# Optimization experiments

Measured on AMD Instinct MI355X. Metric: run time of the kernel, lower is better.

Reference implementation:

```python
import jax, jax.numpy as jnp
import numpy as np


def _safe_norm(x, eps=1e-8):
    return jnp.sqrt(jnp.clip(jnp.sum(x * x, axis=-1, keepdims=True), eps))


def _normalize(x, eps=1e-8):
    return x / _safe_norm(x, eps)


def _safe_direction(primary, fallback, eps=1e-6):
    bad = _safe_norm(primary, eps) < eps  # [N,1] bool
    out = jnp.where(bad, fallback, primary)
    return _normalize(out, eps)


def _build_frames(x):
    # x: [N,3] (N >= 2). Returns per-node rotation frames [N,3,3] (columns = axes).
    d = x[1:] - x[:-1]
    prev = jnp.concatenate([d[:1], d], axis=0)
    nxt = jnp.concatenate([d, d[-1:]], axis=0)
    tangent = _safe_direction(prev + nxt, nxt)
    curvature = _safe_direction(nxt - prev, prev)
    ay_raw = curvature - tangent * jnp.sum(curvature * tangent, axis=-1, keepdims=True)
    ay = _safe_direction(ay_raw, jnp.cross(tangent, prev))
    az = _safe_direction(jnp.cross(tangent, ay), jnp.cross(tangent, curvature))
    ay = _safe_direction(jnp.cross(az, tangent), ay)
    return jnp.stack([tangent, ay, az], axis=-1)


def setup_inputs() -> dict:
    key = jax.random.key(0)
    N, H, EH = 1024, 256, 128  # EH = max(16, H//2)
    ks = jax.random.split(key, 16)

    def lin(k, fi, fo):
        k1, k2 = jax.random.split(k)
        lim = 1.0 / np.sqrt(fi)
        W = jax.random.uniform(k1, (fi, fo), minval=-lim, maxval=lim, dtype=jnp.float32)
        b = jax.random.uniform(k2, (fo,), minval=-lim, maxval=lim, dtype=jnp.float32)
        return W, b

    h = jax.random.normal(ks[0], (N, H), dtype=jnp.float32)
    x_cond = jnp.cumsum(jax.random.normal(ks[1], (N, 3), dtype=jnp.float32) * 1.5, axis=0)
    x_t = x_cond + 0.05 * jax.random.normal(ks[2], (N, 3), dtype=jnp.float32)
    tau = jax.random.uniform(ks[3], (1,), dtype=jnp.float32)
    W_np1, b_np1 = lin(ks[4], H + 6, H)
    W_np2, b_np2 = lin(ks[5], H, H)
    w_src, b_src = lin(ks[6], H, 1)
    w_dst, b_dst = lin(ks[7], H, 1)
    w_ns, b_ns = lin(ks[8], H, 1)
    W_eg1, b_eg1 = lin(ks[9], 4, EH)
    w_eg2, b_eg2 = lin(ks[10], EH, 1)
    W_out1, b_out1 = lin(ks[11], H + 6, H)
    W_out2, b_out2 = lin(ks[12], H, 3)
    return dict(h=h, x_t=x_t, x_cond=x_cond, tau=tau,
                W_np1=W_np1, b_np1=b_np1, W_np2=W_np2, b_np2=b_np2,
                w_src=w_src, b_src=b_src, w_dst=w_dst, b_dst=b_dst,
                w_ns=w_ns, b_ns=b_ns, W_eg1=W_eg1, b_eg1=b_eg1,
                w_eg2=w_eg2, b_eg2=b_eg2, W_out1=W_out1, b_out1=b_out1,
                W_out2=W_out2, b_out2=b_out2)


def reference(h, x_t, x_cond, tau,
              W_np1, b_np1, W_np2, b_np2,
              w_src, b_src, w_dst, b_dst,
              w_ns, b_ns, W_eg1, b_eg1, w_eg2, b_eg2,
              W_out1, b_out1, W_out2, b_out2):
    silu = jax.nn.silu
    n = x_t.shape[0]
    frames = _build_frames(x_cond)                       # [N,3,3]
    delta = x_t - x_cond
    delta_local = jnp.einsum('nji,nj->ni', frames, delta)  # frames^T @ delta
    t = tau.reshape(())
    t_emb = jnp.broadcast_to(jnp.stack([t, jnp.sin(t), jnp.cos(t)]), (n, 3))
    node_feat = jnp.concatenate([h, delta_local, t_emb], axis=-1)
    nh = silu(node_feat @ W_np1 + b_np1)
    nh = silu(nh @ W_np2 + b_np2)                        # [N,H]
    # pairwise local geometry: rel[n,m] = x[m] - x[n], rotated into node n's frame
    rel = x_t[None, :, :] - x_t[:, None, :]              # [N,N,3]
    rel_local = jnp.einsum('nji,nmj->nmi', frames, rel)  # [N,N,3]
    dist = jnp.linalg.norm(rel_local, axis=-1, keepdims=True)
    edge_feat = jnp.concatenate([rel_local, dist], axis=-1)  # [N,N,4]
    eh = silu(edge_feat @ W_eg1 + b_eg1)                 # [N,N,EH]
    edge_logit = (eh @ w_eg2 + b_eg2)[..., 0]            # [N,N]
    src = nh @ w_src + b_src                             # [N,1] -> broadcast over m
    dst = (nh @ w_dst + b_dst)[:, 0]                     # [N]
    logits = src + dst[None, :] + edge_logit             # [N,N]
    diag = jnp.eye(n, dtype=bool)
    logits = jnp.where(diag, -10000.0, logits)
    attn = jax.nn.softmax(logits, axis=1)
    attn = jnp.where(diag, 0.0, attn)
    attn = attn / jnp.clip(jnp.sum(attn, axis=1, keepdims=True), 1e-6)
    ns = jax.nn.sigmoid(nh @ w_ns + b_ns)[:, 0]          # [N]
    msgs = jnp.einsum('nm,m,nmi->ni', attn, ns, rel_local)  # [N,3]
    uf = jnp.concatenate([nh, delta_local, msgs], axis=-1)
    local_update = silu(uf @ W_out1 + b_out1) @ W_out2 + b_out2
    vel_local = local_update + 0.25 * msgs
    return jnp.einsum('nij,nj->ni', frames, vel_local)
```

## Files before the change

### kernel.cpp

```cpp
#include <hip/hip_runtime.h>
#include <math.h>

#define DEV __device__ __forceinline__

typedef float v2f __attribute__((ext_vector_type(2)));
DEV v2f splat2(float s){ return (v2f){s, s}; }

struct F3 { float x, y, z; };

DEV F3 mkf3(float x, float y, float z){ F3 r; r.x=x; r.y=y; r.z=z; return r; }
DEV F3 f3add(F3 a, F3 b){ return mkf3(a.x+b.x, a.y+b.y, a.z+b.z); }
DEV F3 f3sub(F3 a, F3 b){ return mkf3(a.x-b.x, a.y-b.y, a.z-b.z); }
DEV F3 f3scale(F3 a, float s){ return mkf3(a.x*s, a.y*s, a.z*s); }
DEV float f3dot(F3 a, F3 b){ return a.x*b.x + a.y*b.y + a.z*b.z; }
DEV F3 f3cross(F3 a, F3 b){
  return mkf3(a.y*b.z - a.z*b.y, a.z*b.x - a.x*b.z, a.x*b.y - a.y*b.x);
}
DEV F3 f3dir(F3 v){
  float ss = f3dot(v, v);
  float inv = 1.0f / sqrtf(fmaxf(ss, 1e-6f));
  return f3scale(v, inv);
}
DEV float fast_silu(float x){
  return x * __builtin_amdgcn_rcpf(1.0f + __expf(-x));
}
DEV float fast_sigmoid(float x){
  return __builtin_amdgcn_rcpf(1.0f + __expf(-x));
}

__global__ void frames_kernel(const float* __restrict__ xc,
                              const float* __restrict__ xt,
                              float* __restrict__ frames,
                              float* __restrict__ dl,
                              const float* __restrict__ W_eg1,
                              const float* __restrict__ b_eg1,
                              const float* __restrict__ w_eg2,
                              float* __restrict__ wpk, int N)
{
  if (blockIdx.x == (unsigned)(N / 256)) {
    int j = threadIdx.x;
    if (j < 128) {
      const float nl2e = -1.44269504088896340736f;
      const float nln2 = -0.69314718055994530942f;
      wpk[j*8+0] = nl2e * W_eg1[j];
      wpk[j*8+1] = nl2e * W_eg1[128 + j];
      wpk[j*8+2] = nl2e * W_eg1[256 + j];
      wpk[j*8+3] = nl2e * W_eg1[384 + j];
      wpk[j*8+4] = nl2e * b_eg1[j];
      wpk[j*8+5] = nln2 * w_eg2[j];
      wpk[j*8+6] = 0.f; wpk[j*8+7] = 0.f;
    } else if (j < 144) {
      wpk[1024 + (j - 128)] = 0.f;
    }
    return;
  }
  int n = blockIdx.x * blockDim.x + threadIdx.x;
  if (n >= N) return;
  int pn = (n > 0) ? n - 1 : 0;
  int qn = (n < N - 1) ? n : N - 2;
  F3 prev = mkf3(xc[(pn+1)*3+0]-xc[pn*3+0], xc[(pn+1)*3+1]-xc[pn*3+1], xc[(pn+1)*3+2]-xc[pn*3+2]);
  F3 nxt  = mkf3(xc[(qn+1)*3+0]-xc[qn*3+0], xc[(qn+1)*3+1]-xc[qn*3+1], xc[(qn+1)*3+2]-xc[qn*3+2]);

  F3 tangent = f3dir(f3add(prev, nxt));
  F3 curv    = f3dir(f3sub(nxt, prev));
  float ct   = f3dot(curv, tangent);
  F3 ay      = f3dir(f3sub(curv, f3scale(tangent, ct)));
  F3 az      = f3dir(f3cross(tangent, ay));
  ay         = f3dir(f3cross(az, tangent));

  float* fr = frames + n * 9;
  fr[0] = tangent.x; fr[1] = ay.x; fr[2] = az.x;
  fr[3] = tangent.y; fr[4] = ay.y; fr[5] = az.y;
  fr[6] = tangent.z; fr[7] = ay.z; fr[8] = az.z;

  F3 delta = mkf3(xt[n*3+0]-xc[n*3+0], xt[n*3+1]-xc[n*3+1], xt[n*3+2]-xc[n*3+2]);
  dl[n*3+0] = f3dot(tangent, delta);
  dl[n*3+1] = f3dot(ay, delta);
  dl[n*3+2] = f3dot(az, delta);
}

__global__ __launch_bounds__(256) void node_mlp(
    const float* __restrict__ h, const float* __restrict__ dl,
    const float* __restrict__ tau,
    const float* __restrict__ W1, const float* __restrict__ b1,
    const float* __restrict__ W2, const float* __restrict__ b2,
    const float* __restrict__ w_src, const float* __restrict__ b_src,
    const float* __restrict__ w_dst, const float* __restrict__ b_dst,
    const float* __restrict__ w_ns, const float* __restrict__ b_ns,
    float* __restrict__ nh, float* __restrict__ srcv,
    float* __restrict__ dstv, float* __restrict__ nsv, int N)
{
  const int n0 = blockIdx.x * 4, tid = threadIdx.x;
  __shared__ float4 fA[262];
  __shared__ float4 fB[256];
  __shared__ float red[4][4][3];

  {
    const float* hp = h + n0 * 256 + tid;
    fA[tid] = make_float4(hp[0], hp[256], hp[512], hp[768]);
  }
  if (tid < 6) {
    int k = 256 + tid;
    float4 v;
    if (tid < 3) {
      v = make_float4(dl[(n0+0)*3+tid], dl[(n0+1)*3+tid],
                      dl[(n0+2)*3+tid], dl[(n0+3)*3+tid]);
    } else {
      float t = tau[0];
      float s = (tid == 3) ? t : ((tid == 4) ? sinf(t) : cosf(t));
      v = make_float4(s, s, s, s);
    }
    fA[k] = v;
  }
  __syncthreads();

  {
    float bb = b1[tid];
    float a0 = bb, a1 = bb, a2 = bb, a3 = bb;
    const float* Wp = W1 + tid;
    for (int kb = 0; kb < 256; kb += 64) {
      float w[64];
      #pragma unroll
      for (int u = 0; u < 64; ++u) w[u] = Wp[(kb + u) * 256];
      #pragma unroll
      for (int u = 0; u < 64; ++u) {
        float4 f = fA[kb + u];
        a0 = fmaf(f.x, w[u], a0); a1 = fmaf(f.y, w[u], a1);
        a2 = fmaf(f.z, w[u], a2); a3 = fmaf(f.w, w[u], a3);
      }
    }
    #pragma unroll
    for (int k = 256; k < 262; ++k) {
      float w = Wp[k * 256];
      float4 f = fA[k];
      a0 = fmaf(f.x, w, a0); a1 = fmaf(f.y, w, a1);
      a2 = fmaf(f.z, w, a2); a3 = fmaf(f.w, w, a3);
    }
    fB[tid] = make_float4(fast_silu(a0), fast_silu(a1), fast_silu(a2), fast_silu(a3));
  }
  __syncthreads();

  float bb = b2[tid];
  float a0 = bb, a1 = bb, a2 = bb, a3 = bb;
  const float* Wp = W2 + tid;
  for (int kb = 0; kb < 256; kb += 64) {
    float w[64];
    #pragma unroll
    for (int u = 0; u < 64; ++u) w[u] = Wp[(kb + u) * 256];
    #pragma unroll
    for (int u = 0; u < 64; ++u) {
      float4 f = fB[kb + u];
      a0 = fmaf(f.x, w[u], a0); a1 = fmaf(f.y, w[u], a1);
      a2 = fmaf(f.z, w[u], a2); a3 = fmaf(f.w, w[u], a3);
    }
  }

  const float wsv = w_src[tid], wdv = w_dst[tid], wnv = w_ns[tid];
  const int wave = tid >> 6, lane = tid & 63;
  float va[4] = {fast_silu(a0), fast_silu(a1), fast_silu(a2), fast_silu(a3)};
  #pragma unroll
  for (int r = 0; r < 4; ++r) {
    nh[(n0 + r) * 256 + tid] = va[r];
    float ps = va[r] * wsv, pd = va[r] * wdv, pn = va[r] * wnv;
    for (int off = 32; off; off >>= 1) {
      ps += __shfl_down(ps, off);
      pd += __shfl_down(pd, off);
      pn += __shfl_down(pn, off);
    }
    if (lane == 0) { red[wave][r][0] = ps; red[wave][r][1] = pd; red[wave][r][2] = pn; }
  }
  __syncthreads();
  if (tid < 4) {
    int r = tid;
    float s0 = 0.f, s1 = 0.f, s2 = 0.f;
    #pragma unroll
    for (int w = 0; w < 4; ++w) { s0 += red[w][r][0]; s1 += red[w][r][1]; s2 += red[w][r][2]; }
    srcv[n0 + r] = s0 + b_src[0];
    dstv[n0 + r] = s1 + b_dst[0];
    nsv[n0 + r]  = fast_sigmoid(s2 + b_ns[0]);
  }
}

__global__ __launch_bounds__(256) void edge_softmax(
    const float* __restrict__ x_t, const float* __restrict__ frames,
    const float* __restrict__ srcv, const float* __restrict__ dstv,
    const float* __restrict__ nsv,
    const float* __restrict__ wpk, const float* __restrict__ b_eg2,
    float* __restrict__ msgs, int N)
{
  const int n = blockIdx.x, tid = threadIdx.x;
  __shared__ float redmax[4];
  __shared__ float red[4][4];

  const float f0 = frames[n*9+0], f1 = frames[n*9+1], f2 = frames[n*9+2],
              f3_ = frames[n*9+3], f4 = frames[n*9+4], f5 = frames[n*9+5],
              f6 = frames[n*9+6], f7 = frames[n*9+7], f8 = frames[n*9+8];
  const float x0 = x_t[n*3+0], x1 = x_t[n*3+1], x2 = x_t[n*3+2];
  const float sn = srcv[n];
  const float b2v = b_eg2[0];

  float r0s[4], r1s[4], r2s[4], dds[4];
  #pragma unroll
  for (int e = 0; e < 4; ++e) {
    const int m = e * 256 + tid;
    float rx = x_t[m * 3 + 0] - x0;
    float ry = x_t[m * 3 + 1] - x1;
    float rz = x_t[m * 3 + 2] - x2;
    r0s[e] = f0 * rx + f3_ * ry + f6 * rz;
    r1s[e] = f1 * rx + f4 * ry + f7 * rz;
    r2s[e] = f2 * rx + f5 * ry + f8 * rz;
    dds[e] = sqrtf(r0s[e]*r0s[e] + r1s[e]*r1s[e] + r2s[e]*r2s[e]);
  }
  const v2f r0A = {r0s[0], r0s[1]}, r0B = {r0s[2], r0s[3]};
  const v2f r1A = {r1s[0], r1s[1]}, r1B = {r1s[2], r1s[3]};
  const v2f r2A = {r2s[0], r2s[1]}, r2B = {r2s[2], r2s[3]};
  const v2f ddA = {dds[0], dds[1]}, ddB = {dds[2], dds[3]};

  v2f accA = {0.f, 0.f}, accB = {0.f, 0.f};

  const float4* __restrict__ wp4 = (const float4*)wpk;

#define J_STEP(WA, WB)                                                    \
  {                                                                       \
    v2f tpA = splat2(WB.x) + splat2(WA.w) * ddA;                          \
    tpA += splat2(WA.z) * r2A;                                            \
    tpA += splat2(WA.y) * r1A;                                            \
    tpA += splat2(WA.x) * r0A;                                            \
    v2f tpB = splat2(WB.x) + splat2(WA.w) * ddB;                          \
    tpB += splat2(WA.z) * r2B;                                            \
    tpB += splat2(WA.y) * r1B;                                            \
    tpB += splat2(WA.x) * r0B;                                            \
    v2f eA, eB;                                                           \
    eA.x = __builtin_amdgcn_exp2f(tpA.x); eA.y = __builtin_amdgcn_exp2f(tpA.y); \
    eB.x = __builtin_amdgcn_exp2f(tpB.x); eB.y = __builtin_amdgcn_exp2f(tpB.y); \
    v2f opA = eA + splat2(1.0f);                                          \
    v2f opB = eB + splat2(1.0f);                                          \
    v2f sgA, sgB;                                                         \
    sgA.x = __builtin_amdgcn_rcpf(opA.x); sgA.y = __builtin_amdgcn_rcpf(opA.y); \
    sgB.x = __builtin_amdgcn_rcpf(opB.x); sgB.y = __builtin_amdgcn_rcpf(opB.y); \
    accA += (splat2(WB.y) * tpA) * sgA;                                   \
    accB += (splat2(WB.y) * tpB) * sgB;                                   \
  }

  float4 ca0 = wp4[0], cb0 = wp4[1], ca1 = wp4[2], cb1 = wp4[3];
  for (int c = 0; c < 64; ++c) {
    float4 na0 = wp4[(c + 1) * 4 + 0];
    float4 nb0 = wp4[(c + 1) * 4 + 1];
    float4 na1 = wp4[(c + 1) * 4 + 2];
    float4 nb1 = wp4[(c + 1) * 4 + 3];
    J_STEP(ca0, cb0)
    J_STEP(ca1, cb1)
    ca0 = na0; cb0 = nb0; ca1 = na1; cb1 = nb1;
  }
#undef J_STEP

  float l[4];
  float lmax = -3.4e38f;
  float accs[4] = {accA.x, accA.y, accB.x, accB.y};
  #pragma unroll
  for (int e = 0; e < 4; ++e) {
    const int m = e * 256 + tid;
    float lg = sn + dstv[m] + b2v + accs[e];
    if (m == n) lg = -10000.0f;
    l[e] = lg;
    lmax = fmaxf(lmax, lg);
  }

  for (int off = 32; off; off >>= 1) lmax = fmaxf(lmax, __shfl_down(lmax, off));
  const int wave = tid >> 6, lane = tid & 63;
  if (lane == 0) redmax[wave] = lmax;
  __syncthreads();
  const float mx = fmaxf(fmaxf(redmax[0], redmax[1]), fmaxf(redmax[2], redmax[3]));

  float r0all[4] = {r0A.x, r0A.y, r0B.x, r0B.y};
  float r1all[4] = {r1A.x, r1A.y, r1B.x, r1B.y};
  float r2all[4] = {r2A.x, r2A.y, r2B.x, r2B.y};
  float sum = 0.f, a0 = 0.f, a1 = 0.f, a2 = 0.f;
  #pragma unroll
  for (int e = 0; e < 4; ++e) {
    const int m = e * 256 + tid;
    float ee = __expf(l[e] - mx);
    sum += ee;
    float w = ee * nsv[m];
    a0 = fmaf(w, r0all[e], a0);
    a1 = fmaf(w, r1all[e], a1);
    a2 = fmaf(w, r2all[e], a2);
  }
  for (int off = 32; off; off >>= 1) {
    sum += __shfl_down(sum, off);
    a0 += __shfl_down(a0, off);
    a1 += __shfl_down(a1, off);
    a2 += __shfl_down(a2, off);
  }
  if (lane == 0) { red[wave][0] = sum; red[wave][1] = a0; red[wave][2] = a1; red[wave][3] = a2; }
  __syncthreads();
  if (tid == 0) {
    float Z  = red[0][0] + red[1][0] + red[2][0] + red[3][0];
    float m0 = red[0][1] + red[1][1] + red[2][1] + red[3][1];
    float m1 = red[0][2] + red[1][2] + red[2][2] + red[3][2];
    float m2 = red[0][3] + red[1][3] + red[2][3] + red[3][3];
    float invZ = 1.0f / Z;
    msgs[n * 3 + 0] = m0 * invZ;
    msgs[n * 3 + 1] = m1 * invZ;
    msgs[n * 3 + 2] = m2 * invZ;
  }
}

__global__ __launch_bounds__(256) void out_mlp(
    const float* __restrict__ nh, const float* __restrict__ dl,
    const float* __restrict__ msgs, const float* __restrict__ frames,
    const float* __restrict__ W1, const float* __restrict__ b1,
    const float* __restrict__ W2, const float* __restrict__ b2,
    float* __restrict__ out, int N)
{
  const int n0 = blockIdx.x * 4, tid = threadIdx.x;
  __shared__ float4 feat4[262];
  __shared__ float red[4][4][3];
  {
    const float* hp = nh + n0 * 256 + tid;
    feat4[tid] = make_float4(hp[0], hp[256], hp[512], hp[768]);
  }
  if (tid < 6) {
    int k = 256 + tid;
    float4 v;
    if (tid < 3) {
      v = make_float4(dl[(n0+0)*3+tid], dl[(n0+1)*3+tid],
                      dl[(n0+2)*3+tid], dl[(n0+3)*3+tid]);
    } else {
      int c = tid - 3;
      v = make_float4(msgs[(n0+0)*3+c], msgs[(n0+1)*3+c],
                      msgs[(n0+2)*3+c], msgs[(n0+3)*3+c]);
    }
    feat4[k] = v;
  }
  __syncthreads();

  float bb = b1[tid];
  float a0 = bb, a1 = bb, a2 = bb, a3 = bb;
  const float* Wp = W1 + tid;
  for (int kb = 0; kb < 256; kb += 64) {
    float w[64];
    #pragma unroll
    for (int u = 0; u < 64; ++u) w[u] = Wp[(kb + u) * 256];
    #pragma unroll
    for (int u = 0; u < 64; ++u) {
      float4 f = feat4[kb + u];
      a0 = fmaf(f.x, w[u], a0); a1 = fmaf(f.y, w[u], a1);
      a2 = fmaf(f.z, w[u], a2); a3 = fmaf(f.w, w[u], a3);
    }
  }
  #pragma unroll
  for (int k = 256; k < 262; ++k) {
    float w = Wp[k * 256];
    float4 f = feat4[k];
    a0 = fmaf(f.x, w, a0); a1 = fmaf(f.y, w, a1);
    a2 = fmaf(f.z, w, a2); a3 = fmaf(f.w, w, a3);
  }

  const float w0 = W2[tid * 3 + 0], w1 = W2[tid * 3 + 1], w2 = W2[tid * 3 + 2];
  const int wave = tid >> 6, lane = tid & 63;
  float va[4] = {fast_silu(a0), fast_silu(a1), fast_silu(a2), fast_silu(a3)};
  #pragma unroll
  for (int r = 0; r < 4; ++r) {
    float p0 = va[r] * w0, p1 = va[r] * w1, p2 = va[r] * w2;
    for (int off = 32; off; off >>= 1) {
      p0 += __shfl_down(p0, off);
      p1 += __shfl_down(p1, off);
      p2 += __shfl_down(p2, off);
    }
    if (lane == 0) { red[wave][r][0] = p0; red[wave][r][1] = p1; red[wave][r][2] = p2; }
  }
  __syncthreads();
  if (tid < 4) {
    int r = tid, n = n0 + r;
    float s0 = 0.f, s1 = 0.f, s2 = 0.f;
    #pragma unroll
    for (int w = 0; w < 4; ++w) { s0 += red[w][r][0]; s1 += red[w][r][1]; s2 += red[w][r][2]; }
    float m0 = msgs[n * 3 + 0], m1 = msgs[n * 3 + 1], m2 = msgs[n * 3 + 2];
    float v0 = s0 + b2[0] + 0.25f * m0;
    float v1 = s1 + b2[1] + 0.25f * m1;
    float v2 = s2 + b2[2] + 0.25f * m2;
    const float* fr = frames + n * 9;
    out[n * 3 + 0] = fr[0] * v0 + fr[1] * v1 + fr[2] * v2;
    out[n * 3 + 1] = fr[3] * v0 + fr[4] * v1 + fr[5] * v2;
    out[n * 3 + 2] = fr[6] * v0 + fr[7] * v1 + fr[8] * v2;
  }
}

extern "C" void kernel_launch(void* const* d_in, const int* in_sizes, int n_in,
                              void* d_out, int out_size, void* d_ws, size_t ws_size,
                              hipStream_t stream) {
  const float* h      = (const float*)d_in[0];
  const float* x_t    = (const float*)d_in[1];
  const float* x_cond = (const float*)d_in[2];
  const float* tau    = (const float*)d_in[3];
  const float* W_np1  = (const float*)d_in[4];
  const float* b_np1  = (const float*)d_in[5];
  const float* W_np2  = (const float*)d_in[6];
  const float* b_np2  = (const float*)d_in[7];
  const float* w_src  = (const float*)d_in[8];
  const float* b_src  = (const float*)d_in[9];
  const float* w_dst  = (const float*)d_in[10];
  const float* b_dst  = (const float*)d_in[11];
  const float* w_ns   = (const float*)d_in[12];
  const float* b_ns   = (const float*)d_in[13];
  const float* W_eg1  = (const float*)d_in[14];
  const float* b_eg1  = (const float*)d_in[15];
  const float* w_eg2  = (const float*)d_in[16];
  const float* b_eg2  = (const float*)d_in[17];
  const float* W_out1 = (const float*)d_in[18];
  const float* b_out1 = (const float*)d_in[19];
  const float* W_out2 = (const float*)d_in[20];
  const float* b_out2 = (const float*)d_in[21];
  float* out = (float*)d_out;

  const int N = in_sizes[1] / 3;

  float* ws     = (float*)d_ws;
  float* frames = ws;
  float* dl     = frames + N * 9;
  float* nh     = dl + N * 3;
  float* srcv   = nh + N * 256;
  float* dstv   = srcv + N;
  float* nsv    = dstv + N;
  float* msgs   = nsv + N;
  float* wpk    = msgs + N * 3;

  frames_kernel<<<N / 256 + 1, 256, 0, stream>>>(x_cond, x_t, frames, dl,
                                                 W_eg1, b_eg1, w_eg2, wpk, N);
  node_mlp<<<N / 4, 256, 0, stream>>>(h, dl, tau, W_np1, b_np1, W_np2, b_np2,
                                      w_src, b_src, w_dst, b_dst, w_ns, b_ns,
                                      nh, srcv, dstv, nsv, N);
  edge_softmax<<<N, 256, 0, stream>>>(x_t, frames, srcv, dstv, nsv,
                                      wpk, b_eg2, msgs, N);
  out_mlp<<<N / 4, 256, 0, stream>>>(nh, dl, msgs, frames,
                                     W_out1, b_out1, W_out2, b_out2, out, N);
}
```

Baseline: 65.07 us.

## Fuse frame construction and weight packing into node MLP kernel

Removes the separate frames_kernel launch by computing per-node frames and local deltas inside node_mlp (four threads per block) and packing the edge-MLP weights in block 0. The local deltas go through shared memory instead of a global round trip. In edge_softmax, dstv and nsv are loaded early into registers, and the inner loop uses explicit packed FMAs instead of separate multiply and add. This saves one kernel launch and a dependency at the cost of a small serial prologue plus an extra barrier in every node_mlp block.

```diff
diff --git a/kernel.cpp b/kernel.cpp
--- a/kernel.cpp
+++ b/kernel.cpp
@@ -5,6 +5,7 @@
 
 typedef float v2f __attribute__((ext_vector_type(2)));
 DEV v2f splat2(float s){ return (v2f){s, s}; }
+DEV v2f pkfma(v2f a, v2f b, v2f c){ return __builtin_elementwise_fma(a, b, c); }
 
 struct F3 { float x, y, z; };
 
@@ -28,65 +29,18 @@
   return __builtin_amdgcn_rcpf(1.0f + __expf(-x));
 }
 
-__global__ void frames_kernel(const float* __restrict__ xc,
-                              const float* __restrict__ xt,
-                              float* __restrict__ frames,
-                              float* __restrict__ dl,
-                              const float* __restrict__ W_eg1,
-                              const float* __restrict__ b_eg1,
-                              const float* __restrict__ w_eg2,
-                              float* __restrict__ wpk, int N)
-{
-  if (blockIdx.x == (unsigned)(N / 256)) {
-    int j = threadIdx.x;
-    if (j < 128) {
-      const float nl2e = -1.44269504088896340736f;
-      const float nln2 = -0.69314718055994530942f;
-      wpk[j*8+0] = nl2e * W_eg1[j];
-      wpk[j*8+1] = nl2e * W_eg1[128 + j];
-      wpk[j*8+2] = nl2e * W_eg1[256 + j];
-      wpk[j*8+3] = nl2e * W_eg1[384 + j];
-      wpk[j*8+4] = nl2e * b_eg1[j];
-      wpk[j*8+5] = nln2 * w_eg2[j];
-      wpk[j*8+6] = 0.f; wpk[j*8+7] = 0.f;
-    } else if (j < 144) {
-      wpk[1024 + (j - 128)] = 0.f;
-    }
-    return;
-  }
-  int n = blockIdx.x * blockDim.x + threadIdx.x;
-  if (n >= N) return;
-  int pn = (n > 0) ? n - 1 : 0;
-  int qn = (n < N - 1) ? n : N - 2;
-  F3 prev = mkf3(xc[(pn+1)*3+0]-xc[pn*3+0], xc[(pn+1)*3+1]-xc[pn*3+1], xc[(pn+1)*3+2]-xc[pn*3+2]);
-  F3 nxt  = mkf3(xc[(qn+1)*3+0]-xc[qn*3+0], xc[(qn+1)*3+1]-xc[qn*3+1], xc[(qn+1)*3+2]-xc[qn*3+2]);
-
-  F3 tangent = f3dir(f3add(prev, nxt));
-  F3 curv    = f3dir(f3sub(nxt, prev));
-  float ct   = f3dot(curv, tangent);
-  F3 ay      = f3dir(f3sub(curv, f3scale(tangent, ct)));
-  F3 az      = f3dir(f3cross(tangent, ay));
-  ay         = f3dir(f3cross(az, tangent));
-
-  float* fr = frames + n * 9;
-  fr[0] = tangent.x; fr[1] = ay.x; fr[2] = az.x;
-  fr[3] = tangent.y; fr[4] = ay.y; fr[5] = az.y;
-  fr[6] = tangent.z; fr[7] = ay.z; fr[8] = az.z;
-
-  F3 delta = mkf3(xt[n*3+0]-xc[n*3+0], xt[n*3+1]-xc[n*3+1], xt[n*3+2]-xc[n*3+2]);
-  dl[n*3+0] = f3dot(tangent, delta);
-  dl[n*3+1] = f3dot(ay, delta);
-  dl[n*3+2] = f3dot(az, delta);
-}
-
 __global__ __launch_bounds__(256) void node_mlp(
-    const float* __restrict__ h, const float* __restrict__ dl,
-    const float* __restrict__ tau,
+    const float* __restrict__ h, const float* __restrict__ xc,
+    const float* __restrict__ xt, const float* __restrict__ tau,
     const float* __restrict__ W1, const float* __restrict__ b1,
     const float* __restrict__ W2, const float* __restrict__ b2,
     const float* __restrict__ w_src, const float* __restrict__ b_src,
     const float* __restrict__ w_dst, const float* __restrict__ b_dst,
     const float* __restrict__ w_ns, const float* __restrict__ b_ns,
+    const float* __restrict__ W_eg1, const float* __restrict__ b_eg1,
+    const float* __restrict__ w_eg2,
+    float* __restrict__ frames, float* __restrict__ dl,
+    float* __restrict__ wpk,
     float* __restrict__ nh, float* __restrict__ srcv,
     float* __restrict__ dstv, float* __restrict__ nsv, int N)
 {
@@ -94,6 +48,47 @@
   __shared__ float4 fA[262];
   __shared__ float4 fB[256];
   __shared__ float red[4][4][3];
+  __shared__ float sdl[4][3];
+
+  if (blockIdx.x == 0 && tid >= 128) {
+    int j = tid - 128;
+    const float nl2e = -1.44269504088896340736f;
+    const float nln2 = -0.69314718055994530942f;
+    wpk[j*8+0] = nl2e * W_eg1[j];
+    wpk[j*8+1] = nl2e * W_eg1[128 + j];
+    wpk[j*8+2] = nl2e * W_eg1[256 + j];
+    wpk[j*8+3] = nl2e * W_eg1[384 + j];
+    wpk[j*8+4] = nl2e * b_eg1[j];
+    wpk[j*8+5] = nln2 * w_eg2[j];
+    wpk[j*8+6] = 0.f; wpk[j*8+7] = 0.f;
+    if (j < 16) wpk[1024 + j] = 0.f;
+  }
+
+  if (tid < 4) {
+    int n = n0 + tid;
+    int pn = (n > 0) ? n - 1 : 0;
+    int qn = (n < N - 1) ? n : N - 2;
+    F3 prev = mkf3(xc[(pn+1)*3+0]-xc[pn*3+0], xc[(pn+1)*3+1]-xc[pn*3+1], xc[(pn+1)*3+2]-xc[pn*3+2]);
+    F3 nxt  = mkf3(xc[(qn+1)*3+0]-xc[qn*3+0], xc[(qn+1)*3+1]-xc[qn*3+1], xc[(qn+1)*3+2]-xc[qn*3+2]);
+
+    F3 tangent = f3dir(f3add(prev, nxt));
+    F3 curv    = f3dir(f3sub(nxt, prev));
+    float ct   = f3dot(curv, tangent);
+    F3 ay      = f3dir(f3sub(curv, f3scale(tangent, ct)));
+    F3 az      = f3dir(f3cross(tangent, ay));
+    ay         = f3dir(f3cross(az, tangent));
+
+    float* fr = frames + n * 9;
+    fr[0] = tangent.x; fr[1] = ay.x; fr[2] = az.x;
+    fr[3] = tangent.y; fr[4] = ay.y; fr[5] = az.y;
+    fr[6] = tangent.z; fr[7] = ay.z; fr[8] = az.z;
+
+    F3 delta = mkf3(xt[n*3+0]-xc[n*3+0], xt[n*3+1]-xc[n*3+1], xt[n*3+2]-xc[n*3+2]);
+    float d0 = f3dot(tangent, delta), d1 = f3dot(ay, delta), d2 = f3dot(az, delta);
+    dl[n*3+0] = d0; dl[n*3+1] = d1; dl[n*3+2] = d2;
+    sdl[tid][0] = d0; sdl[tid][1] = d1; sdl[tid][2] = d2;
+  }
+  __syncthreads();
 
   {
     const float* hp = h + n0 * 256 + tid;
@@ -103,8 +98,7 @@
     int k = 256 + tid;
     float4 v;
     if (tid < 3) {
-      v = make_float4(dl[(n0+0)*3+tid], dl[(n0+1)*3+tid],
-                      dl[(n0+2)*3+tid], dl[(n0+3)*3+tid]);
+      v = make_float4(sdl[0][tid], sdl[1][tid], sdl[2][tid], sdl[3][tid]);
     } else {
       float t = tau[0];
       float s = (tid == 3) ? t : ((tid == 4) ? sinf(t) : cosf(t));
@@ -199,10 +193,12 @@
   const float sn = srcv[n];
   const float b2v = b_eg2[0];
 
-  float r0s[4], r1s[4], r2s[4], dds[4];
+  float r0s[4], r1s[4], r2s[4], dds[4], dst_r[4], ns_r[4];
   #pragma unroll
   for (int e = 0; e < 4; ++e) {
     const int m = e * 256 + tid;
+    dst_r[e] = dstv[m];
+    ns_r[e]  = nsv[m];
     float rx = x_t[m * 3 + 0] - x0;
     float ry = x_t[m * 3 + 1] - x1;
     float rz = x_t[m * 3 + 2] - x2;
@@ -220,26 +216,29 @@
 
   const float4* __restrict__ wp4 = (const float4*)wpk;
 
-#define J_STEP(WA, WB)                                                    \
-  {                                                                       \
-    v2f tpA = splat2(WB.x) + splat2(WA.w) * ddA;                          \
-    tpA += splat2(WA.z) * r2A;                                            \
-    tpA += splat2(WA.y) * r1A;                                            \
-    tpA += splat2(WA.x) * r0A;                                            \
-    v2f tpB = splat2(WB.x) + splat2(WA.w) * ddB;                          \
-    tpB += splat2(WA.z) * r2B;                                            \
-    tpB += splat2(WA.y) * r1B;                                            \
-    tpB += splat2(WA.x) * r0B;                                            \
-    v2f eA, eB;                                                           \
+#define J_STEP(WA, WB)                                                        \
+  {                                                                           \
+    v2f wxx = splat2(WA.x), wyy = splat2(WA.y);                               \
+    v2f wzz = splat2(WA.z), wdd = splat2(WA.w);                               \
+    v2f wbb = splat2(WB.x), w22 = splat2(WB.y);                               \
+    v2f tpA = pkfma(wdd, ddA, wbb);                                           \
+    tpA = pkfma(wzz, r2A, tpA);                                               \
+    tpA = pkfma(wyy, r1A, tpA);                                               \
+    tpA = pkfma(wxx, r0A, tpA);                                               \
+    v2f tpB = pkfma(wdd, ddB, wbb);                                           \
+    tpB = pkfma(wzz, r2B, tpB);                                               \
+    tpB = pkfma(wyy, r1B, tpB);                                               \
+    tpB = pkfma(wxx, r0B, tpB);                                               \
+    v2f eA, eB;                                                               \
     eA.x = __builtin_amdgcn_exp2f(tpA.x); eA.y = __builtin_amdgcn_exp2f(tpA.y); \
     eB.x = __builtin_amdgcn_exp2f(tpB.x); eB.y = __builtin_amdgcn_exp2f(tpB.y); \
-    v2f opA = eA + splat2(1.0f);                                          \
-    v2f opB = eB + splat2(1.0f);                                          \
-    v2f sgA, sgB;                                                         \
+    v2f opA = eA + splat2(1.0f);                                              \
+    v2f opB = eB + splat2(1.0f);                                              \
+    v2f sgA, sgB;                                                             \
     sgA.x = __builtin_amdgcn_rcpf(opA.x); sgA.y = __builtin_amdgcn_rcpf(opA.y); \
     sgB.x = __builtin_amdgcn_rcpf(opB.x); sgB.y = __builtin_amdgcn_rcpf(opB.y); \
-    accA += (splat2(WB.y) * tpA) * sgA;                                   \
-    accB += (splat2(WB.y) * tpB) * sgB;                                   \
+    accA = pkfma(w22 * tpA, sgA, accA);                                       \
+    accB = pkfma(w22 * tpB, sgB, accB);                                       \
   }
 
   float4 ca0 = wp4[0], cb0 = wp4[1], ca1 = wp4[2], cb1 = wp4[3];
@@ -260,7 +259,7 @@
   #pragma unroll
   for (int e = 0; e < 4; ++e) {
     const int m = e * 256 + tid;
-    float lg = sn + dstv[m] + b2v + accs[e];
+    float lg = sn + dst_r[e] + b2v + accs[e];
     if (m == n) lg = -10000.0f;
     l[e] = lg;
     lmax = fmaxf(lmax, lg);
@@ -278,10 +277,9 @@
   float sum = 0.f, a0 = 0.f, a1 = 0.f, a2 = 0.f;
   #pragma unroll
   for (int e = 0; e < 4; ++e) {
-    const int m = e * 256 + tid;
     float ee = __expf(l[e] - mx);
     sum += ee;
-    float w = ee * nsv[m];
+    float w = ee * ns_r[e];
     a0 = fmaf(w, r0all[e], a0);
     a1 = fmaf(w, r1all[e], a1);
     a2 = fmaf(w, r2all[e], a2);
@@ -426,10 +424,11 @@
   float* msgs   = nsv + N;
   float* wpk    = msgs + N * 3;
 
-  frames_kernel<<<N / 256 + 1, 256, 0, stream>>>(x_cond, x_t, frames, dl,
-                                                 W_eg1, b_eg1, w_eg2, wpk, N);
-  node_mlp<<<N / 4, 256, 0, stream>>>(h, dl, tau, W_np1, b_np1, W_np2, b_np2,
+  node_mlp<<<N / 4, 256, 0, stream>>>(h, x_cond, x_t, tau,
+                                      W_np1, b_np1, W_np2, b_np2,
                                       w_src, b_src, w_dst, b_dst, w_ns, b_ns,
+                                      W_eg1, b_eg1, w_eg2,
+                                      frames, dl, wpk,
                                       nh, srcv, dstv, nsv, N);
   edge_softmax<<<N, 256, 0, stream>>>(x_t, frames, srcv, dstv, nsv,
                                       wpk, b_eg2, msgs, N);
```

Measured after the change: 61.93 us (median of 2 runs). -4.8%, faster.
